# Performance work log

Measured on AMD Instinct MI355X. Metric: run time of the kernel, lower is better.

## Reference

```python
import jax, jax.numpy as jnp
import numpy as np

H = 128   # hidden_dim
E = 768   # embedding_dim
L = 20    # num_layers
B = 64    # batch
T = 512   # seq_len


def setup_inputs() -> dict:
    key = jax.random.key(0)
    ks = jax.random.split(key, 9)
    k = 1.0 / np.sqrt(H)  # PyTorch LSTM default init scale
    u = lambda kk, shape: jax.random.uniform(kk, shape, jnp.float32, -k, k)
    return {
        "x": jax.random.normal(ks[0], (B, T, E), jnp.float32),
        "Wih0": u(ks[1], (4 * H, E)),        # layer 0 input weights
        "Whh0": u(ks[2], (4 * H, H)),
        "bih0": u(ks[3], (4 * H,)),
        "bhh0": u(ks[4], (4 * H,)),
        "Wih": u(ks[5], (L - 1, 4 * H, H)),  # layers 1..19
        "Whh": u(ks[6], (L - 1, 4 * H, H)),
        "bih": u(ks[7], (L - 1, 4 * H)),
        "bhh": u(ks[8], (L - 1, 4 * H)),
    }


def _lstm_layer(xs, Wih, Whh, b):
    # xs: [T, B, Din] -> ys: [T, B, H], h_final: [B, H]
    bsz = xs.shape[1]
    pre = jnp.einsum('tbd,gd->tbg', xs, Wih) + b  # precompute input projections

    def step(carry, pt):
        h, c = carry
        g = pt + h @ Whh.T  # [B, 4H]
        i, f, gg, o = jnp.split(g, 4, axis=-1)  # PyTorch gate order i,f,g,o
        i = jax.nn.sigmoid(i)
        f = jax.nn.sigmoid(f)
        gg = jnp.tanh(gg)
        o = jax.nn.sigmoid(o)
        c = f * c + i * gg
        h = o * jnp.tanh(c)
        return (h, c), h

    init = (jnp.zeros((bsz, H), xs.dtype), jnp.zeros((bsz, H), xs.dtype))
    (_, _), ys = jax.lax.scan(step, init, pre)
    return ys, ys[-1]


def reference(x, Wih0, Whh0, bih0, bhh0, Wih, Whh, bih, bhh):
    xs = jnp.swapaxes(x, 0, 1)  # [T, B, E]
    ys, _ = _lstm_layer(xs, Wih0, Whh0, bih0 + bhh0)

    def layer_fn(ys, params):
        Wl, Wh, bi, bh = params
        ys2, h = _lstm_layer(ys, Wl, Wh, bi + bh)
        return ys2, h

    ys, hs = jax.lax.scan(layer_fn, ys, (Wih, Whh, bih, bhh))
    return hs[-1]  # hidden state of last (20th) layer at final timestep: [B, H]
```

## Files before the change

### kernel.cpp

```cpp
#include <hip/hip_runtime.h>

#define H4 128
#define EE 768
#define NL 20
#define BB 64
#define TT 512
#define G4 512
#define NBG 8
#define CK 16
#define NCH (TT/CK)
#define RC 2
#define HB 131072

typedef _Float16 v8h __attribute__((ext_vector_type(8)));
typedef _Float16 v4h __attribute__((ext_vector_type(4)));
typedef float v4f __attribute__((ext_vector_type(4)));
typedef unsigned int v4u __attribute__((ext_vector_type(4)));

#if defined(__has_builtin)
#if __has_builtin(__builtin_amdgcn_exp2f) && __has_builtin(__builtin_amdgcn_rcpf)
#define EXP2F __builtin_amdgcn_exp2f
#define RCPF  __builtin_amdgcn_rcpf
#endif
#endif
#ifndef EXP2F
#define EXP2F exp2f
#define RCPF(x) (1.0f/(x))
#endif

__device__ __forceinline__ float fast_sig(float x) {
  float e = EXP2F(-1.44269504f * x);
  return RCPF(1.0f + e);
}
__device__ __forceinline__ float fast_tanh(float x) {
  float e = EXP2F(2.88539008f * x);
  return 1.0f - 2.0f * RCPF(1.0f + e);
}

__device__ __forceinline__ int swz(int row, int byteInRow) {
  return (row * 256 + byteInRow) ^ ((row & 7) << 4);
}

__global__ __launch_bounds__(256) void prep_kernel(
    const float* __restrict__ Wih0, const float* __restrict__ Whh0,
    const float* __restrict__ bih,  const float* __restrict__ bhh,
    const float* __restrict__ Wih,  const float* __restrict__ Whh,
    _Float16* __restrict__ W0h, _Float16* __restrict__ Wc,
    float* __restrict__ biasc, unsigned* __restrict__ flags)
{
  long idx = (long)blockIdx.x * 256 + threadIdx.x;
  const long NWC = (long)NL * G4 * 256;
  const long NW0 = (long)G4 * EE;
  const long NBI = (long)NL * G4;
  if (idx < NWC) {
    int l = (int)(idx >> 17);
    int rem = (int)(idx & 131071);
    int n = rem >> 8, kk = rem & 255;
    float v;
    if (l == 0) v = (kk < 128) ? 0.0f : Whh0[n * H4 + kk - 128];
    else v = (kk < 128) ? Wih[((long)(l-1) * G4 + n) * H4 + kk]
                        : Whh[((long)(l-1) * G4 + n) * H4 + kk - 128];
    Wc[idx] = (_Float16)v;
  } else if ((idx -= NWC) < NW0) {
    W0h[idx] = (_Float16)Wih0[idx];
  } else if ((idx -= NW0) < NBI) {
    int l = (int)(idx >> 9), n = (int)(idx & 511);
    biasc[idx] = (l == 0) ? 0.0f : (bih[(l-1) * G4 + n] + bhh[(l-1) * G4 + n]);
  } else if ((idx -= NBI) < 256) {
    flags[idx] = 0u;
  }
}

__global__ __launch_bounds__(512) void pre0_gemm(
    const float* __restrict__ x, const _Float16* __restrict__ W0h,
    const float* __restrict__ bih0, const float* __restrict__ bhh0,
    _Float16* __restrict__ pre0)
{
  __shared__ __align__(16) unsigned char smem[46080];
  _Float16* sA = (_Float16*)smem;
  _Float16* sB = (_Float16*)(smem + 5120);
  _Float16* sC = (_Float16*)smem;
  int t = blockIdx.x;
  int tid = threadIdx.x;
  int w = tid >> 6, lane = tid & 63;
  int l15 = lane & 15, kb = lane >> 4;

  v4f acc[4][4];
#pragma unroll
  for (int mi = 0; mi < 4; ++mi)
#pragma unroll
    for (int ni = 0; ni < 4; ++ni) acc[mi][ni] = (v4f){0.f, 0.f, 0.f, 0.f};

  int bA = tid >> 3, kqA = tid & 7;
  const float* xp = x + ((long)bA * TT + t) * EE + kqA * 4;
  const _Float16* wp = W0h + (long)tid * EE;

  for (int k0 = 0; k0 < EE; k0 += 32) {
    float4 xv = *(const float4*)(xp + k0);
    v4h xh = { (_Float16)xv.x, (_Float16)xv.y, (_Float16)xv.z, (_Float16)xv.w };
    *(v4h*)&sA[bA * 40 + kqA * 4] = xh;
#pragma unroll
    for (int c = 0; c < 4; ++c)
      *(v8h*)&sB[tid * 40 + c * 8] = *(const v8h*)(wp + k0 + c * 8);
    __syncthreads();
#pragma unroll
    for (int mi = 0; mi < 4; ++mi) {
      v8h a = *(const v8h*)&sA[(16 * mi + l15) * 40 + kb * 8];
#pragma unroll
      for (int ni = 0; ni < 4; ++ni) {
        v8h b = *(const v8h*)&sB[(64 * w + 16 * ni + l15) * 40 + kb * 8];
        acc[mi][ni] = __builtin_amdgcn_mfma_f32_16x16x32_f16(a, b, acc[mi][ni], 0, 0, 0);
      }
    }
    __syncthreads();
  }

#pragma unroll
  for (int hh2 = 0; hh2 < 2; ++hh2) {
    __syncthreads();
    if ((w >> 2) == hh2) {
      int wl = w & 3;
#pragma unroll
      for (int ni = 0; ni < 4; ++ni) {
        int nloc = 64 * wl + 16 * ni + l15;
        int n = 256 * hh2 + nloc;
        float bia = bih0[n] + bhh0[n];
#pragma unroll
        for (int mi = 0; mi < 4; ++mi)
#pragma unroll
          for (int r = 0; r < 4; ++r)
            sC[nloc * 72 + 16 * mi + 4 * kb + r] = (_Float16)(acc[mi][ni][r] + bia);
      }
    }
    __syncthreads();
    int row = tid >> 1, part = tid & 1;
    int n = 256 * hh2 + row;
#pragma unroll
    for (int g = 0; g < 4; ++g) {
      int bg = part * 4 + g;
      _Float16* po = pre0 + (((long)t * 8 + bg) * 512 + n) * 8;
      *(v8h*)po = *(const v8h*)&sC[row * 72 + part * 32 + g * 8];
    }
  }
}

__global__ __launch_bounds__(512, 1) void lstm_pipe(
    const _Float16* __restrict__ pre0, const _Float16* __restrict__ Wc,
    const float* __restrict__ biasc, _Float16* __restrict__ yring,
    unsigned* __restrict__ flags, float* __restrict__ out)
{
  __shared__ __align__(16) unsigned char lds[HB + 8192];
  const int l = blockIdx.x >> 3, bg = blockIdx.x & 7;
  const int tid = threadIdx.x, w = tid >> 6, lane = tid & 63;
  const int l15 = lane & 15, kb = lane >> 4;
  const int jloc = 16 * w + l15;
  const bool valid = (kb < 2);
  const int b0 = 4 * (kb & 1);

  v8h bw[4][8];
  const _Float16* wbase = Wc + (long)l * G4 * 256;
#pragma unroll
  for (int q = 0; q < 4; ++q)
#pragma unroll
    for (int ks = 0; ks < 8; ++ks)
      bw[q][ks] = *(const v8h*)(wbase + (long)(128 * q + jloc) * 256 + ks * 32 + kb * 8);

  float bias_q[4];
#pragma unroll
  for (int q = 0; q < 4; ++q)
    bias_q[q] = (l == 0) ? 0.0f : biasc[l * G4 + 128 * q + jloc];

  *(v4u*)(lds + HB + tid * 16) = (v4u){0u, 0u, 0u, 0u};

  const int myf = l * 8 + bg;
  const unsigned* fin  = flags + ((l > 0) ? (myf - 8) : myf);
  const unsigned* fout = flags + ((l < NL - 1) ? (myf + 8) : myf);
  unsigned* fme = flags + myf;
  char* ywr = (char*)(yring + (long)myf * (RC * CK * 1024));
  const char* yrd = (const char*)(yring + (long)(myf - 8) * (RC * CK * 1024));
  const char* pre0b = (const char*)pre0;

  v4f cst = (v4f){0.f, 0.f, 0.f, 0.f};

  __syncthreads();

  for (int c = 0; c < NCH; ++c) {
    if (l > 0) {
      unsigned f;
      for (;;) {
        asm volatile("global_load_dword %0, %1, off sc0 sc1\n\ts_waitcnt vmcnt(0)"
                     : "=v"(f) : "v"(fin));
        if (f > (unsigned)c) break;
        __builtin_amdgcn_s_sleep(2);
      }
      const char* src = yrd + (long)(c & (RC - 1)) * 32768 + tid * 16;
      v4u d0, d1, d2, d3;
      asm volatile("global_load_dwordx4 %0, %1, off sc0 sc1" : "=v"(d0) : "v"(src));
      asm volatile("global_load_dwordx4 %0, %1, off sc0 sc1" : "=v"(d1) : "v"(src + 8192));
      asm volatile("global_load_dwordx4 %0, %1, off sc0 sc1" : "=v"(d2) : "v"(src + 16384));
      asm volatile("global_load_dwordx4 %0, %1, off sc0 sc1" : "=v"(d3) : "v"(src + 24576));
      asm volatile("s_waitcnt vmcnt(0)" ::: "memory");
      __builtin_amdgcn_sched_barrier(0);
      unsigned char* dst = lds + tid * 16;
      *(v4u*)(dst)         = d0;
      *(v4u*)(dst +  8192) = d1;
      *(v4u*)(dst + 16384) = d2;
      *(v4u*)(dst + 24576) = d3;
    } else {
      v4u d[16];
#pragma unroll
      for (int ts = 0; ts < CK; ++ts) {
        const char* s = pre0b + ((long)(c * CK + ts) * 8 + bg) * 8192 + tid * 16;
        d[ts] = *(const v4u*)s;
      }
#pragma unroll
      for (int ts = 0; ts < CK; ++ts)
        *(v4u*)(lds + ts * 8192 + tid * 16) = d[ts];
    }
    if (l < NL - 1 && c >= RC) {
      unsigned f;
      for (;;) {
        asm volatile("global_load_dword %0, %1, off sc0 sc1\n\ts_waitcnt vmcnt(0)"
                     : "=v"(f) : "v"(fout));
        if (f >= (unsigned)(c - 1)) break;
        __builtin_amdgcn_s_sleep(2);
      }
    }
    asm volatile("s_waitcnt lgkmcnt(0)" ::: "memory");
    __builtin_amdgcn_s_barrier();
    __builtin_amdgcn_sched_barrier(0);

    for (int ts = 0; ts < CK; ++ts) {
      const int t = c * CK + ts;
      const int p = t & 1;
      v4f acc[4];
#pragma unroll
      for (int q = 0; q < 4; ++q)
        acc[q] = (v4f){bias_q[q], bias_q[q], bias_q[q], bias_q[q]};

      const unsigned char* hb = lds + HB + p * 4096;
      if (l == 0) {
        const unsigned char* pbts = lds + ts * 8192 + (kb & 1) * 8;
#pragma unroll
        for (int q = 0; q < 4; ++q) {
          v4h pv = *(const v4h*)(pbts + (128 * q + jloc) * 16);
#pragma unroll
          for (int r = 0; r < 4; ++r) acc[q][r] += (float)pv[r];
        }
      } else {
        const unsigned char* yb = lds + ts * 2048;
#pragma unroll
        for (int ks = 0; ks < 4; ++ks) {
          v8h a = *(const v8h*)(yb + swz(l15, ks * 64 + kb * 16));
#pragma unroll
          for (int q = 0; q < 4; ++q)
            acc[q] = __builtin_amdgcn_mfma_f32_16x16x32_f16(a, bw[q][ks], acc[q], 0, 0, 0);
        }
      }
#pragma unroll
      for (int ks = 4; ks < 8; ++ks) {
        v8h a = *(const v8h*)(hb + swz(l15, (ks - 4) * 64 + kb * 16));
#pragma unroll
        for (int q = 0; q < 4; ++q)
          acc[q] = __builtin_amdgcn_mfma_f32_16x16x32_f16(a, bw[q][ks], acc[q], 0, 0, 0);
      }

      _Float16 hh[4]; float hf[4];
#pragma unroll
      for (int r = 0; r < 4; ++r) {
        float i_ = fast_sig(acc[0][r]);
        float f_ = fast_sig(acc[1][r]);
        float g_ = fast_tanh(acc[2][r]);
        float o_ = fast_sig(acc[3][r]);
        float cn = f_ * cst[r] + i_ * g_;
        cst[r] = cn;
        float h_ = o_ * fast_tanh(cn);
        hf[r] = h_; hh[r] = (_Float16)h_;
      }

      if (valid) {
        unsigned char* hn = lds + HB + (p ^ 1) * 4096;
#pragma unroll
        for (int r = 0; r < 4; ++r)
          *(_Float16*)(hn + swz(b0 + r, jloc * 2)) = hh[r];
        if (l == NL - 1 && t == TT - 1) {
#pragma unroll
          for (int r = 0; r < 4; ++r)
            out[(bg * 8 + b0 + r) * H4 + jloc] = hf[r];
        }
      }

      asm volatile("s_waitcnt lgkmcnt(0)" ::: "memory");
      __builtin_amdgcn_s_barrier();
      __builtin_amdgcn_sched_barrier(0);

      if (l < NL - 1) {
        unsigned hv = *(const unsigned*)(lds + HB + (p ^ 1) * 4096 + tid * 4);
        char* dst = ywr + (long)(c & (RC - 1)) * 32768 + ts * 2048 + tid * 4;
        asm volatile("global_store_dword %0, %1, off sc0 sc1" :: "v"(dst), "v"(hv));
      }
    }

    asm volatile("s_waitcnt vmcnt(0)" ::: "memory");
    __builtin_amdgcn_s_barrier();
    __builtin_amdgcn_sched_barrier(0);
    if (tid == 0) {
      unsigned v = (unsigned)(c + 1);
      asm volatile("global_store_dword %0, %1, off sc0 sc1" :: "v"(fme), "v"(v) : "memory");
    }
  }
}

extern "C" void kernel_launch(void* const* d_in, const int* in_sizes, int n_in,
                              void* d_out, int out_size, void* d_ws, size_t ws_size,
                              hipStream_t stream)
{
  const float* x    = (const float*)d_in[0];
  const float* Wih0 = (const float*)d_in[1];
  const float* Whh0 = (const float*)d_in[2];
  const float* bih0 = (const float*)d_in[3];
  const float* bhh0 = (const float*)d_in[4];
  const float* Wih  = (const float*)d_in[5];
  const float* Whh  = (const float*)d_in[6];
  const float* bih  = (const float*)d_in[7];
  const float* bhh  = (const float*)d_in[8];
  float* out = (float*)d_out;
  char* ws = (char*)d_ws;

  _Float16* pre0  = (_Float16*)(ws);
  _Float16* W0h   = (_Float16*)(ws + 33554432);
  _Float16* Wc    = (_Float16*)(ws + 34340864);
  float*    bc    = (float*)   (ws + 39583744);
  _Float16* yring = (_Float16*)(ws + 39624704);
  unsigned* flags = (unsigned*)(ws + 50110464);

  prep_kernel<<<11817, 256, 0, stream>>>(Wih0, Whh0, bih, bhh, Wih, Whh, W0h, Wc, bc, flags);
  pre0_gemm<<<TT, 512, 0, stream>>>(x, W0h, bih0, bhh0, pre0);
  lstm_pipe<<<NL * NBG, 512, 0, stream>>>(pre0, Wc, bc, yring, flags, out);
}
```

Before: 1.072 ms.

## Split input and recurrent MFMA chains, prefetch next step's input projection, split gate math

Each step's MFMA work is split into an input-projection part (accA) and a recurrent part (accB). The input part for step ts+1 is computed after step ts's gate math, which takes it off the serial dependency chain. Gate nonlinearities are now spread across all four lane groups via a cross-lane shuffle, so each lane handles two batch rows instead of four with half the lanes idle. Chunk size is halved and ring depth doubled (CK 8, RC 4) to shrink LDS staging and let producers run further ahead. The price is extra shuffles, more registers held live and more flag synchronisations per sequence.

```diff
diff --git a/kernel.cpp b/kernel.cpp
--- a/kernel.cpp
+++ b/kernel.cpp
@@ -7,10 +7,10 @@
 #define TT 512
 #define G4 512
 #define NBG 8
-#define CK 16
+#define CK 8
 #define NCH (TT/CK)
-#define RC 2
-#define HB 131072
+#define RC 4
+#define HB 65536
 
 typedef _Float16 v8h __attribute__((ext_vector_type(8)));
 typedef _Float16 v4h __attribute__((ext_vector_type(4)));
@@ -154,8 +154,8 @@
   const int tid = threadIdx.x, w = tid >> 6, lane = tid & 63;
   const int l15 = lane & 15, kb = lane >> 4;
   const int jloc = 16 * w + l15;
-  const bool valid = (kb < 2);
-  const int b0 = 4 * (kb & 1);
+  const bool lo = (kb < 2);
+  const int rp = (kb & 1) * 2 + (kb >> 1);
 
   v8h bw[4][8];
   const _Float16* wbase = Wc + (long)l * G4 * 256;
@@ -180,7 +180,7 @@
   const char* yrd = (const char*)(yring + (long)(myf - 8) * (RC * CK * 1024));
   const char* pre0b = (const char*)pre0;
 
-  v4f cst = (v4f){0.f, 0.f, 0.f, 0.f};
+  float c0 = 0.f, c1 = 0.f;
 
   __syncthreads();
 
@@ -193,21 +193,16 @@
         if (f > (unsigned)c) break;
         __builtin_amdgcn_s_sleep(2);
       }
-      const char* src = yrd + (long)(c & (RC - 1)) * 32768 + tid * 16;
-      v4u d0, d1, d2, d3;
+      const char* src = yrd + (long)(c & (RC - 1)) * (CK * 2048) + tid * 32;
+      v4u d0, d1;
       asm volatile("global_load_dwordx4 %0, %1, off sc0 sc1" : "=v"(d0) : "v"(src));
-      asm volatile("global_load_dwordx4 %0, %1, off sc0 sc1" : "=v"(d1) : "v"(src + 8192));
-      asm volatile("global_load_dwordx4 %0, %1, off sc0 sc1" : "=v"(d2) : "v"(src + 16384));
-      asm volatile("global_load_dwordx4 %0, %1, off sc0 sc1" : "=v"(d3) : "v"(src + 24576));
+      asm volatile("global_load_dwordx4 %0, %1, off sc0 sc1" : "=v"(d1) : "v"(src + 16));
       asm volatile("s_waitcnt vmcnt(0)" ::: "memory");
       __builtin_amdgcn_sched_barrier(0);
-      unsigned char* dst = lds + tid * 16;
-      *(v4u*)(dst)         = d0;
-      *(v4u*)(dst +  8192) = d1;
-      *(v4u*)(dst + 16384) = d2;
-      *(v4u*)(dst + 24576) = d3;
+      *(v4u*)(lds + tid * 32)      = d0;
+      *(v4u*)(lds + tid * 32 + 16) = d1;
     } else {
-      v4u d[16];
+      v4u d[CK];
 #pragma unroll
       for (int ts = 0; ts < CK; ++ts) {
         const char* s = pre0b + ((long)(c * CK + ts) * 8 + bg) * 8192 + tid * 16;
@@ -222,7 +217,7 @@
       for (;;) {
         asm volatile("global_load_dword %0, %1, off sc0 sc1\n\ts_waitcnt vmcnt(0)"
                      : "=v"(f) : "v"(fout));
-        if (f >= (unsigned)(c - 1)) break;
+        if (f >= (unsigned)(c - RC + 1)) break;
         __builtin_amdgcn_s_sleep(2);
       }
     }
@@ -230,73 +225,106 @@
     __builtin_amdgcn_s_barrier();
     __builtin_amdgcn_sched_barrier(0);
 
+    v8h yf[4];
+    unsigned pr[4];
+    v4f accA[4];
+    if (l > 0) {
+#pragma unroll
+      for (int ks = 0; ks < 4; ++ks)
+        yf[ks] = *(const v8h*)(lds + swz(l15, ks * 64 + kb * 16));
+#pragma unroll
+      for (int q = 0; q < 4; ++q) {
+        accA[q] = (v4f){bias_q[q], bias_q[q], bias_q[q], bias_q[q]};
+#pragma unroll
+        for (int ks = 0; ks < 4; ++ks)
+          accA[q] = __builtin_amdgcn_mfma_f32_16x16x32_f16(yf[ks], bw[q][ks], accA[q], 0, 0, 0);
+      }
+    } else {
+#pragma unroll
+      for (int q = 0; q < 4; ++q)
+        pr[q] = *(const unsigned*)(lds + (128 * q + jloc) * 16 + rp * 4);
+    }
+
     for (int ts = 0; ts < CK; ++ts) {
       const int t = c * CK + ts;
       const int p = t & 1;
-      v4f acc[4];
-#pragma unroll
-      for (int q = 0; q < 4; ++q)
-        acc[q] = (v4f){bias_q[q], bias_q[q], bias_q[q], bias_q[q]};
-
       const unsigned char* hb = lds + HB + p * 4096;
+
+      v4f accB[4];
+#pragma unroll
+      for (int q = 0; q < 4; ++q) accB[q] = (v4f){0.f, 0.f, 0.f, 0.f};
+#pragma unroll
+      for (int ks = 0; ks < 4; ++ks) {
+        v8h hf = *(const v8h*)(hb + swz(l15, ks * 64 + kb * 16));
+#pragma unroll
+        for (int q = 0; q < 4; ++q)
+          accB[q] = __builtin_amdgcn_mfma_f32_16x16x32_f16(hf, bw[q][ks + 4], accB[q], 0, 0, 0);
+      }
+
+      float w0[4], w1[4];
+#pragma unroll
+      for (int q = 0; q < 4; ++q) {
+        v4f s = (l > 0) ? (accA[q] + accB[q]) : accB[q];
+        float t2 = __shfl_xor(s[2], 32);
+        float t3 = __shfl_xor(s[3], 32);
+        w0[q] = lo ? s[0] : t2;
+        w1[q] = lo ? s[1] : t3;
+      }
       if (l == 0) {
-        const unsigned char* pbts = lds + ts * 8192 + (kb & 1) * 8;
 #pragma unroll
         for (int q = 0; q < 4; ++q) {
-          v4h pv = *(const v4h*)(pbts + (128 * q + jloc) * 16);
-#pragma unroll
-          for (int r = 0; r < 4; ++r) acc[q][r] += (float)pv[r];
+          union { unsigned u; _Float16 h[2]; } uu; uu.u = pr[q];
+          w0[q] += (float)uu.h[0];
+          w1[q] += (float)uu.h[1];
         }
-      } else {
-        const unsigned char* yb = lds + ts * 2048;
-#pragma unroll
-        for (int ks = 0; ks < 4; ++ks) {
-          v8h a = *(const v8h*)(yb + swz(l15, ks * 64 + kb * 16));
+      }
+
+      float i0 = fast_sig(w0[0]), ff0 = fast_sig(w0[1]);
+      float g0 = fast_tanh(w0[2]), o0 = fast_sig(w0[3]);
+      c0 = ff0 * c0 + i0 * g0;
+      float h0 = o0 * fast_tanh(c0);
+      float i1 = fast_sig(w1[0]), ff1 = fast_sig(w1[1]);
+      float g1 = fast_tanh(w1[2]), o1 = fast_sig(w1[3]);
+      c1 = ff1 * c1 + i1 * g1;
+      float h1 = o1 * fast_tanh(c1);
+
+      unsigned char* hn = lds + HB + (p ^ 1) * 4096;
+      *(_Float16*)(hn + swz(2 * rp,     jloc * 2)) = (_Float16)h0;
+      *(_Float16*)(hn + swz(2 * rp + 1, jloc * 2)) = (_Float16)h1;
+      if (l == NL - 1 && t == TT - 1) {
+        out[(bg * 8 + 2 * rp) * H4 + jloc]     = h0;
+        out[(bg * 8 + 2 * rp + 1) * H4 + jloc] = h1;
+      }
+
+      if (ts < CK - 1) {
+        if (l > 0) {
+          const unsigned char* yb = lds + (ts + 1) * 2048;
+#pragma unroll
+          for (int ks = 0; ks < 4; ++ks)
+            yf[ks] = *(const v8h*)(yb + swz(l15, ks * 64 + kb * 16));
+#pragma unroll
+          for (int q = 0; q < 4; ++q) {
+            accA[q] = (v4f){bias_q[q], bias_q[q], bias_q[q], bias_q[q]};
+#pragma unroll
+            for (int ks = 0; ks < 4; ++ks)
+              accA[q] = __builtin_amdgcn_mfma_f32_16x16x32_f16(yf[ks], bw[q][ks], accA[q], 0, 0, 0);
+          }
+        } else {
+          const unsigned char* pb = lds + (ts + 1) * 8192;
 #pragma unroll
           for (int q = 0; q < 4; ++q)
-            acc[q] = __builtin_amdgcn_mfma_f32_16x16x32_f16(a, bw[q][ks], acc[q], 0, 0, 0);
+            pr[q] = *(const unsigned*)(pb + (128 * q + jloc) * 16 + rp * 4);
         }
       }
-#pragma unroll
-      for (int ks = 4; ks < 8; ++ks) {
-        v8h a = *(const v8h*)(hb + swz(l15, (ks - 4) * 64 + kb * 16));
-#pragma unroll
-        for (int q = 0; q < 4; ++q)
-          acc[q] = __builtin_amdgcn_mfma_f32_16x16x32_f16(a, bw[q][ks], acc[q], 0, 0, 0);
-      }
-
-      _Float16 hh[4]; float hf[4];
-#pragma unroll
-      for (int r = 0; r < 4; ++r) {
-        float i_ = fast_sig(acc[0][r]);
-        float f_ = fast_sig(acc[1][r]);
-        float g_ = fast_tanh(acc[2][r]);
-        float o_ = fast_sig(acc[3][r]);
-        float cn = f_ * cst[r] + i_ * g_;
-        cst[r] = cn;
-        float h_ = o_ * fast_tanh(cn);
-        hf[r] = h_; hh[r] = (_Float16)h_;
-      }
-
-      if (valid) {
-        unsigned char* hn = lds + HB + (p ^ 1) * 4096;
-#pragma unroll
-        for (int r = 0; r < 4; ++r)
-          *(_Float16*)(hn + swz(b0 + r, jloc * 2)) = hh[r];
-        if (l == NL - 1 && t == TT - 1) {
-#pragma unroll
-          for (int r = 0; r < 4; ++r)
-            out[(bg * 8 + b0 + r) * H4 + jloc] = hf[r];
-        }
-      }
 
       asm volatile("s_waitcnt lgkmcnt(0)" ::: "memory");
+      __builtin_amdgcn_sched_barrier(0);
       __builtin_amdgcn_s_barrier();
       __builtin_amdgcn_sched_barrier(0);
 
       if (l < NL - 1) {
         unsigned hv = *(const unsigned*)(lds + HB + (p ^ 1) * 4096 + tid * 4);
-        char* dst = ywr + (long)(c & (RC - 1)) * 32768 + ts * 2048 + tid * 4;
+        char* dst = ywr + (long)(c & (RC - 1)) * (CK * 2048) + ts * 2048 + tid * 4;
         asm volatile("global_store_dword %0, %1, off sc0 sc1" :: "v"(dst), "v"(hv));
       }
     }
```

After: 978.6 us. -8.8%, faster.
